# Kernel tuning notes

Hardware: AMD Instinct MI355X
Metric: run time of the kernel (lower is better)

Reference implementation:

```python
import jax, jax.numpy as jnp
import numpy as np


def setup_inputs() -> dict:
    key = jax.random.key(0)
    k1, k2 = jax.random.split(key)
    x = jax.random.normal(k1, (32, 128, 56, 56), dtype=jnp.float32)
    weight = jax.random.normal(k2, (256, 128, 3, 3), dtype=jnp.float32) * 0.01
    bias = jnp.zeros((256,), dtype=jnp.float32)
    return {"x": x, "weight": weight, "bias": bias}


def reference(x, weight, bias):
    # Faithful to Conv2dGEMM: im2col + GEMM is mathematically a standard
    # cross-correlation conv with the given stride/padding. We express it as
    # the efficient fused form (implicit GEMM) which computes identical math.
    stride, padding = 1, 1
    out = jax.lax.conv_general_dilated(
        x, weight,
        window_strides=(stride, stride),
        padding=[(padding, padding), (padding, padding)],
        dimension_numbers=("NCHW", "OIHW", "NCHW"),
    )  # [B, out_ch, H_out, W_out]
    return out + bias[None, :, None, None]
```

## Files before the change

kernel.cpp:

```cpp
#include <hip/hip_runtime.h>
#include <stdint.h>

typedef __bf16 bf16x8 __attribute__((ext_vector_type(8)));
typedef __bf16 bf16x4 __attribute__((ext_vector_type(4)));
typedef float  f32x4  __attribute__((ext_vector_type(4)));

#define NB   32
#define CI   128
#define HH   56
#define WW   56
#define CO   256
#define HP   58
#define HW   (HH*WW)
#define MTOT (NB*HW)
#define KTOT 1152

#define XT_ELEMS ((size_t)NB*HP*HP*CI)
#define XT_BYTES (XT_ELEMS*2)

__global__ void zero_kernel(int4* __restrict__ p, int n16) {
  int i = blockIdx.x * blockDim.x + threadIdx.x;
  if (i < n16) p[i] = make_int4(0, 0, 0, 0);
}

__global__ void xpose_kernel(const float* __restrict__ x, __bf16* __restrict__ xt) {
  int nh = blockIdx.x;
  int n = nh / HH, h = nh % HH;
  __shared__ float tile[CI * 57];
  const float* src = x + (size_t)n * CI * HW + (size_t)h * WW;
  int t = threadIdx.x;
  for (int idx = t; idx < CI * WW; idx += 256) {
    int c = idx / WW, w = idx - c * WW;
    tile[c * 57 + w] = src[(size_t)c * HW + w];
  }
  __syncthreads();
  __bf16* dst = xt + ((size_t)(n * HP + h + 1) * HP + 1) * CI;
  for (int idx = t; idx < WW * 32; idx += 256) {
    int w = idx >> 5, c4 = (idx & 31) * 4;
    bf16x4 v;
    v[0] = (__bf16)tile[(c4 + 0) * 57 + w];
    v[1] = (__bf16)tile[(c4 + 1) * 57 + w];
    v[2] = (__bf16)tile[(c4 + 2) * 57 + w];
    v[3] = (__bf16)tile[(c4 + 3) * 57 + w];
    *(bf16x4*)(dst + (size_t)w * CI + c4) = v;
  }
}

__global__ void wxform_kernel(const float* __restrict__ wg, __bf16* __restrict__ wt) {
  int id = blockIdx.x * 256 + threadIdx.x;
  int o = id / KTOT;
  int k = id - o * KTOT;
  int rs = k >> 7, c = k & 127;
  wt[id] = (__bf16)wg[(size_t)o * KTOT + c * 9 + rs];
}

#define BM 128
#define BN 128
#define BK 32

__device__ __forceinline__ void gload_lds16(const __bf16* g, __bf16* l) {
  __builtin_amdgcn_global_load_lds(
      (const __attribute__((address_space(1))) void*)g,
      (__attribute__((address_space(3))) void*)l, 16, 0, 0);
}

__global__ __launch_bounds__(256) void conv_gemm(
    const __bf16* __restrict__ xt, const __bf16* __restrict__ wt,
    const float* __restrict__ bias, float* __restrict__ out) {
  __shared__ __bf16 Alds[BM * BK];
  __shared__ __bf16 Blds[BN * BK];
  int t = threadIdx.x;
  int bx = blockIdx.x;
  int nb = bx & 1, mb = bx >> 1;

  size_t baseA[2], baseB[2];
  __bf16 *ldsA[2], *ldsB[2];
  for (int i = 0; i < 2; ++i) {
    int ml = i * 64 + (t >> 2);
    unsigned m = mb * BM + ml;
    unsigned nimg = m / HW;
    unsigned hw = m - nimg * HW;
    unsigned h = hw / WW;
    unsigned w = hw - h * WW;
    baseA[i] = ((size_t)(nimg * HP + h) * HP + w) * CI + (t & 3) * 8;
    baseB[i] = (size_t)(nb * BN + ml) * KTOT + (t & 3) * 8;
    ldsA[i] = &Alds[(size_t)ml * BK + (t & 3) * 8];
    ldsB[i] = &Blds[(size_t)ml * BK + (t & 3) * 8];
  }

  int wid = t >> 6, lane = t & 63;
  int wm = (wid >> 1) * 64, wn = (wid & 1) * 64;
  int lr = lane & 15, lk = (lane >> 4) * 8;

  const bf16x8* Af[4];
  const bf16x8* Bf[4];
  for (int i = 0; i < 4; ++i) {
    Af[i] = (const bf16x8*)&Alds[(wm + i * 16 + lr) * BK + lk];
    Bf[i] = (const bf16x8*)&Blds[(wn + i * 16 + lr) * BK + lk];
  }

  f32x4 acc[4][4];
  for (int i = 0; i < 4; ++i)
    for (int j = 0; j < 4; ++j) acc[i][j] = (f32x4){0.f, 0.f, 0.f, 0.f};

  for (int kt = 0; kt < KTOT / BK; ++kt) {
    int rs = kt >> 2;
    int r = (rs * 11) >> 5;
    int s = rs - 3 * r;
    size_t offA = ((size_t)(r * HP + s)) * CI + (size_t)(kt & 3) * 32;
    size_t offB = (size_t)kt * BK;
    gload_lds16(xt + baseA[0] + offA, ldsA[0]);
    gload_lds16(xt + baseA[1] + offA, ldsA[1]);
    gload_lds16(wt + baseB[0] + offB, ldsB[0]);
    gload_lds16(wt + baseB[1] + offB, ldsB[1]);
    __syncthreads();
    bf16x8 a[4], b[4];
    for (int i = 0; i < 4; ++i) { a[i] = *Af[i]; b[i] = *Bf[i]; }
    for (int i = 0; i < 4; ++i)
      for (int j = 0; j < 4; ++j)
        acc[i][j] = __builtin_amdgcn_mfma_f32_16x16x32_bf16(a[i], b[j], acc[i][j], 0, 0, 0);
    __syncthreads();
  }

  for (int j = 0; j < 4; ++j) {
    int o = nb * BN + wn + j * 16 + lr;
    float bv = bias[o];
    for (int i = 0; i < 4; ++i) {
      unsigned m0 = mb * BM + wm + i * 16 + (lane >> 4) * 4;
      for (int r2 = 0; r2 < 4; ++r2) {
        unsigned m = m0 + r2;
        unsigned nimg = m / HW;
        unsigned hw = m - nimg * HW;
        out[((size_t)nimg * CO + o) * HW + hw] = acc[i][j][r2] + bv;
      }
    }
  }
}

extern "C" void kernel_launch(void* const* d_in, const int* in_sizes, int n_in,
                              void* d_out, int out_size, void* d_ws, size_t ws_size,
                              hipStream_t stream) {
  const float* x    = (const float*)d_in[0];
  const float* wg   = (const float*)d_in[1];
  const float* bias = (const float*)d_in[2];
  float* out = (float*)d_out;

  __bf16* xt = (__bf16*)d_ws;
  __bf16* wt = (__bf16*)((char*)d_ws + XT_BYTES);

  int n16 = (int)(XT_BYTES / 16);
  zero_kernel<<<(n16 + 255) / 256, 256, 0, stream>>>((int4*)d_ws, n16);
  xpose_kernel<<<NB * HH, 256, 0, stream>>>(x, xt);
  wxform_kernel<<<(CO * KTOT) / 256, 256, 0, stream>>>(wg, wt);
  conv_gemm<<<(MTOT / BM) * (CO / BN), 256, 0, stream>>>(xt, wt, bias, out);
}
```

Baseline: 237.6 us.

## Zero only halo, vectorize transpose, and double K-step per barrier in conv GEMM

Replaces the full-buffer zeroing of the padded NHWC workspace with a kernel that writes only the halo border pixels, which removes a large redundant write. The transpose kernel now reads x with float4 loads and writes 8-wide bf16 vectors. The GEMM main loop handles 64 K elements per iteration using two 32-wide LDS slices, halving the number of barrier pairs, and adds a launch_bounds occupancy hint of 3 blocks. LDS per block doubles, and the two slices are a wider K step rather than true double buffering, so load/compute overlap is unchanged.

```diff
diff --git a/kernel.cpp b/kernel.cpp
--- a/kernel.cpp
+++ b/kernel.cpp
@@ -2,7 +2,6 @@
 #include <stdint.h>
 
 typedef __bf16 bf16x8 __attribute__((ext_vector_type(8)));
-typedef __bf16 bf16x4 __attribute__((ext_vector_type(4)));
 typedef float  f32x4  __attribute__((ext_vector_type(4)));
 
 #define NB   32
@@ -18,31 +17,42 @@
 #define XT_ELEMS ((size_t)NB*HP*HP*CI)
 #define XT_BYTES (XT_ELEMS*2)
 
-__global__ void zero_kernel(int4* __restrict__ p, int n16) {
-  int i = blockIdx.x * blockDim.x + threadIdx.x;
-  if (i < n16) p[i] = make_int4(0, 0, 0, 0);
+__global__ void halo_zero(__bf16* __restrict__ xt) {
+  int id = blockIdx.x * 256 + threadIdx.x;
+  if (id >= NB * 228 * 16) return;
+  int chunk = id & 15;
+  int p = (id >> 4) % 228;
+  int n = id / (228 * 16);
+  int h, w;
+  if (p < 58)       { h = 0;           w = p; }
+  else if (p < 116) { h = 57;          w = p - 58; }
+  else if (p < 172) { h = p - 116 + 1; w = 0; }
+  else              { h = p - 172 + 1; w = 57; }
+  int4* dst = (int4*)(xt + ((size_t)(n * HP + h) * HP + w) * CI) + chunk;
+  *dst = make_int4(0, 0, 0, 0);
 }
 
 __global__ void xpose_kernel(const float* __restrict__ x, __bf16* __restrict__ xt) {
   int nh = blockIdx.x;
   int n = nh / HH, h = nh % HH;
-  __shared__ float tile[CI * 57];
+  __shared__ float tile[CI][57];
   const float* src = x + (size_t)n * CI * HW + (size_t)h * WW;
   int t = threadIdx.x;
-  for (int idx = t; idx < CI * WW; idx += 256) {
-    int c = idx / WW, w = idx - c * WW;
-    tile[c * 57 + w] = src[(size_t)c * HW + w];
+  for (int idx = t; idx < CI * 14; idx += 256) {
+    int c = idx / 14, w4 = idx - c * 14;
+    float4 v = *(const float4*)(src + (size_t)c * HW + w4 * 4);
+    tile[c][w4 * 4 + 0] = v.x;
+    tile[c][w4 * 4 + 1] = v.y;
+    tile[c][w4 * 4 + 2] = v.z;
+    tile[c][w4 * 4 + 3] = v.w;
   }
   __syncthreads();
   __bf16* dst = xt + ((size_t)(n * HP + h + 1) * HP + 1) * CI;
-  for (int idx = t; idx < WW * 32; idx += 256) {
-    int w = idx >> 5, c4 = (idx & 31) * 4;
-    bf16x4 v;
-    v[0] = (__bf16)tile[(c4 + 0) * 57 + w];
-    v[1] = (__bf16)tile[(c4 + 1) * 57 + w];
-    v[2] = (__bf16)tile[(c4 + 2) * 57 + w];
-    v[3] = (__bf16)tile[(c4 + 3) * 57 + w];
-    *(bf16x4*)(dst + (size_t)w * CI + c4) = v;
+  for (int idx = t; idx < WW * 16; idx += 256) {
+    int w = idx >> 4, c8 = (idx & 15) * 8;
+    bf16x8 v;
+    for (int k = 0; k < 8; ++k) v[k] = (__bf16)tile[c8 + k][w];
+    *(bf16x8*)(dst + (size_t)w * CI + c8) = v;
   }
 }
 
@@ -56,7 +66,6 @@
 
 #define BM 128
 #define BN 128
-#define BK 32
 
 __device__ __forceinline__ void gload_lds16(const __bf16* g, __bf16* l) {
   __builtin_amdgcn_global_load_lds(
@@ -64,17 +73,18 @@
       (__attribute__((address_space(3))) void*)l, 16, 0, 0);
 }
 
-__global__ __launch_bounds__(256) void conv_gemm(
+__global__ __launch_bounds__(256, 3) void conv_gemm(
     const __bf16* __restrict__ xt, const __bf16* __restrict__ wt,
     const float* __restrict__ bias, float* __restrict__ out) {
-  __shared__ __bf16 Alds[BM * BK];
-  __shared__ __bf16 Blds[BN * BK];
+  __shared__ __bf16 Alds[2][BM * 32];
+  __shared__ __bf16 Blds[2][BN * 32];
   int t = threadIdx.x;
   int bx = blockIdx.x;
   int nb = bx & 1, mb = bx >> 1;
 
   size_t baseA[2], baseB[2];
-  __bf16 *ldsA[2], *ldsB[2];
+  __bf16* ldsA[2][2];
+  __bf16* ldsB[2][2];
   for (int i = 0; i < 2; ++i) {
     int ml = i * 64 + (t >> 2);
     unsigned m = mb * BM + ml;
@@ -84,41 +94,43 @@
     unsigned w = hw - h * WW;
     baseA[i] = ((size_t)(nimg * HP + h) * HP + w) * CI + (t & 3) * 8;
     baseB[i] = (size_t)(nb * BN + ml) * KTOT + (t & 3) * 8;
-    ldsA[i] = &Alds[(size_t)ml * BK + (t & 3) * 8];
-    ldsB[i] = &Blds[(size_t)ml * BK + (t & 3) * 8];
+    for (int p = 0; p < 2; ++p) {
+      ldsA[i][p] = &Alds[p][ml * 32 + (t & 3) * 8];
+      ldsB[i][p] = &Blds[p][ml * 32 + (t & 3) * 8];
+    }
   }
 
   int wid = t >> 6, lane = t & 63;
   int wm = (wid >> 1) * 64, wn = (wid & 1) * 64;
   int lr = lane & 15, lk = (lane >> 4) * 8;
 
-  const bf16x8* Af[4];
-  const bf16x8* Bf[4];
-  for (int i = 0; i < 4; ++i) {
-    Af[i] = (const bf16x8*)&Alds[(wm + i * 16 + lr) * BK + lk];
-    Bf[i] = (const bf16x8*)&Blds[(wn + i * 16 + lr) * BK + lk];
-  }
-
   f32x4 acc[4][4];
   for (int i = 0; i < 4; ++i)
     for (int j = 0; j < 4; ++j) acc[i][j] = (f32x4){0.f, 0.f, 0.f, 0.f};
 
-  for (int kt = 0; kt < KTOT / BK; ++kt) {
-    int rs = kt >> 2;
+  for (int kt = 0; kt < KTOT / 64; ++kt) {
+    int rs = kt >> 1;
     int r = (rs * 11) >> 5;
     int s = rs - 3 * r;
-    size_t offA = ((size_t)(r * HP + s)) * CI + (size_t)(kt & 3) * 32;
-    size_t offB = (size_t)kt * BK;
-    gload_lds16(xt + baseA[0] + offA, ldsA[0]);
-    gload_lds16(xt + baseA[1] + offA, ldsA[1]);
-    gload_lds16(wt + baseB[0] + offB, ldsB[0]);
-    gload_lds16(wt + baseB[1] + offB, ldsB[1]);
+    size_t offA = ((size_t)(r * HP + s)) * CI + (size_t)(kt & 1) * 64;
+    size_t offB = (size_t)kt * 64;
+    for (int p = 0; p < 2; ++p) {
+      gload_lds16(xt + baseA[0] + offA + p * 32, ldsA[0][p]);
+      gload_lds16(xt + baseA[1] + offA + p * 32, ldsA[1][p]);
+      gload_lds16(wt + baseB[0] + offB + p * 32, ldsB[0][p]);
+      gload_lds16(wt + baseB[1] + offB + p * 32, ldsB[1][p]);
+    }
     __syncthreads();
-    bf16x8 a[4], b[4];
-    for (int i = 0; i < 4; ++i) { a[i] = *Af[i]; b[i] = *Bf[i]; }
-    for (int i = 0; i < 4; ++i)
-      for (int j = 0; j < 4; ++j)
-        acc[i][j] = __builtin_amdgcn_mfma_f32_16x16x32_bf16(a[i], b[j], acc[i][j], 0, 0, 0);
+    for (int p = 0; p < 2; ++p) {
+      bf16x8 a[4], b[4];
+      for (int i = 0; i < 4; ++i) {
+        a[i] = *(const bf16x8*)&Alds[p][(wm + i * 16 + lr) * 32 + lk];
+        b[i] = *(const bf16x8*)&Blds[p][(wn + i * 16 + lr) * 32 + lk];
+      }
+      for (int i = 0; i < 4; ++i)
+        for (int j = 0; j < 4; ++j)
+          acc[i][j] = __builtin_amdgcn_mfma_f32_16x16x32_bf16(a[i], b[j], acc[i][j], 0, 0, 0);
+    }
     __syncthreads();
   }
 
@@ -148,8 +160,7 @@
   __bf16* xt = (__bf16*)d_ws;
   __bf16* wt = (__bf16*)((char*)d_ws + XT_BYTES);
 
-  int n16 = (int)(XT_BYTES / 16);
-  zero_kernel<<<(n16 + 255) / 256, 256, 0, stream>>>((int4*)d_ws, n16);
+  halo_zero<<<(NB * 228 * 16 + 255) / 256, 256, 0, stream>>>(xt);
   xpose_kernel<<<NB * HH, 256, 0, stream>>>(x, xt);
   wxform_kernel<<<(CO * KTOT) / 256, 256, 0, stream>>>(wg, wt);
   conv_gemm<<<(MTOT / BM) * (CO / BN), 256, 0, stream>>>(xt, wt, bias, out);
```

Result: faster. 225.0 us (-5.3%).
